# Kernel optimization log

Hardware: AMD Instinct MI355X
Metric: run time of the kernel (lower is better)

Reference implementation:

```python
import jax, jax.numpy as jnp
import numpy as np
from functools import partial

FRAME_RATE = 100
MIN_BPM = 55.0
MAX_BPM = 215.0
THRESHOLD = 0.05
TRANSITION_LAMBDA = 100.0  # madmom-style exponential tempo-change penalty
NEG = jnp.float32(-1e9)


def _build_dbn():
    """Bar-pointer DBN: one block of `tau` phase states per tempo interval tau."""
    min_int = int(round(60.0 * FRAME_RATE / MAX_BPM))
    max_int = int(round(60.0 * FRAME_RATE / MIN_BPM))
    intervals = np.arange(min_int, max_int + 1)              # (T_tempi,)
    state_positions = np.concatenate([np.arange(t) for t in intervals])  # (S,)
    first_idx = np.cumsum(intervals) - intervals             # pos-0 state per tempo
    last_idx = np.cumsum(intervals) - 1                      # last state per tempo
    # exponential tempo-transition distribution, row-normalized in log space
    ratio = intervals[None, :].astype(np.float64) / intervals[:, None]
    raw = -TRANSITION_LAMBDA * np.abs(ratio - 1.0)
    trans_log = raw - np.log(np.exp(raw - raw.max(1, keepdims=True)).sum(1, keepdims=True)) - raw.max(1, keepdims=True)
    return (
        jnp.asarray(state_positions == 0),                    # pos0_mask (S,) bool
        jnp.asarray(first_idx, dtype=jnp.int32),
        jnp.asarray(last_idx, dtype=jnp.int32),
        jnp.asarray(trans_log, dtype=jnp.float32),            # (T_tempi, T_tempi)
    )


def setup_inputs() -> dict:
    key = jax.random.key(0)
    logit = jax.random.normal(key, (4, 6000), dtype=jnp.float32)
    return {"logit": logit}


@jax.jit
def reference(logit):
    pos0_mask, first_idx, last_idx, trans_log = _build_dbn()
    S = pos0_mask.shape[0]
    B, T = logit.shape

    beat_lp = jax.nn.log_sigmoid(logit)      # (B, T)
    nonbeat_lp = jax.nn.log_sigmoid(-logit)  # (B, T)

    def emission(b_t, nb_t):
        # (B, S): beat log-prob on phase-0 states, non-beat elsewhere
        return jnp.where(pos0_mask[None, :], b_t[:, None], nb_t[:, None])

    # ---- Viterbi forward pass with backpointers ----
    def step(delta, xs):
        b_t, nb_t = xs
        prev_last = delta[:, last_idx]                         # (B, T_tempi)
        cand = prev_last[:, :, None] + trans_log[None, :, :]   # (B, from, to)
        from_beat = cand.max(axis=1)                           # (B, T_tempi)
        bp_beat = last_idx[cand.argmax(axis=1)]                # (B, T_tempi)
        # within-tempo advance: state s comes from s-1 (blocks are contiguous)
        shifted = jnp.concatenate(
            [jnp.full((B, 1), NEG, delta.dtype), delta[:, :-1]], axis=1)
        combined = shifted.at[:, first_idx].set(from_beat)
        new_delta = combined + emission(b_t, nb_t)
        bp = jnp.broadcast_to(jnp.arange(S, dtype=jnp.int32) - 1, (B, S))
        bp = bp.at[:, first_idx].set(bp_beat)
        return new_delta, bp

    delta0 = emission(beat_lp[:, 0], nonbeat_lp[:, 0]) - jnp.log(jnp.float32(S))
    xs = (beat_lp[:, 1:].T, nonbeat_lp[:, 1:].T)               # each (T-1, B)
    delta_final, bps = jax.lax.scan(step, delta0, xs)          # bps: (T-1, B, S)

    # ---- backtrack ----
    final_state = jnp.argmax(delta_final, axis=1).astype(jnp.int32)  # (B,)

    def back(state, bp_t):
        prev = jnp.take_along_axis(bp_t, state[:, None], axis=1)[:, 0]
        return prev, state

    state0, ys = jax.lax.scan(back, final_state, bps, reverse=True)
    path = jnp.concatenate([state0[None, :], ys], axis=0)      # (T, B) state ids

    on_beat = pos0_mask[path].T                                # (B, T)
    act = jax.nn.sigmoid(logit)
    beat_mask = on_beat & (act >= jnp.float32(THRESHOLD))
    return beat_mask.astype(jnp.float32)                       # 1.0 at beat frames
```

## Files before the change

### kernel.cpp

```cpp
#include <hip/hip_runtime.h>
#include <math.h>

#define NTAU 82
#define TMIN 28
#define S_TOT 5617
#define TF 6000
#define BATCH 4
#define WMAX 28
#define AP 84
#define NTHREADS 1024
#define NCHUNK 215
#define CHUNK_F (WMAX * AP)
#define NPOS 41

#define TRANS_OFF 0
#define BLP_OFF   8192
#define NBLP_OFF  32768
#define AH_OFF    57344
#define FLAG_OFF  (AH_OFF + BATCH * NCHUNK * CHUNK_F)
#define RESV_OFF  (FLAG_OFF + 16)
#define RESI_OFF  (RESV_OFF + 8)

typedef float v2f __attribute__((ext_vector_type(2)));

__device__ __forceinline__ int first_of(int b) { return b * (55 + b) / 2; }

__device__ __forceinline__ float logsig(float x) {
    return -(fmaxf(-x, 0.0f) + log1pf(expf(-fabsf(x))));
}

__global__ void k_trans(float* __restrict__ ws) {
    int i = blockIdx.x;
    int j = threadIdx.x;
    __shared__ double sh[128];
    double raw = 0.0, e = 0.0;
    double ti = 28.0 + (double)i;
    if (j < NTAU) {
        double tj = 28.0 + (double)j;
        raw = -100.0 * fabs(tj / ti - 1.0);
        e = exp(raw);
    }
    sh[j] = e;
    __syncthreads();
    for (int st = 64; st > 0; st >>= 1) {
        if (j < st) sh[j] += sh[j + st];
        __syncthreads();
    }
    double lse = log(sh[0]);
    if (j < NTAU) ws[TRANS_OFF + i * NTAU + j] = (float)(raw - lse);
}

__global__ void k_emis(const float* __restrict__ logit, float* __restrict__ ws,
                       float* __restrict__ out) {
    int idx = blockIdx.x * blockDim.x + threadIdx.x;
    if (idx < BATCH * TF) {
        float x = logit[idx];
        ws[BLP_OFF + idx]  = logsig(x);
        ws[NBLP_OFF + idx] = logsig(-x);
        out[idx] = 0.0f;
    }
}

__global__ void k_flags(int* __restrict__ flags) {
    if (threadIdx.x < 16) flags[threadIdx.x] = 0;
}

__global__ __attribute__((amdgpu_flat_work_group_size(NTHREADS, NTHREADS),
                          amdgpu_waves_per_eu(4, 4),
                          amdgpu_num_vgpr(128)))
void k_viterbi(const float* __restrict__ logit,
               const float* __restrict__ transg,
               const float* __restrict__ blp_all,
               const float* __restrict__ nblp_all,
               float* __restrict__ Ah_all,
               int*   __restrict__ flags,
               float* __restrict__ resv,
               int*   __restrict__ resi,
               float* __restrict__ out) {
    const int tid = threadIdx.x;
    const int b   = blockIdx.x >> 1;
    const int h   = blockIdx.x & 1;

    const float* blp  = blp_all  + b * TF;
    const float* nblp = nblp_all + b * TF;
    float* Ah = Ah_all + (size_t)b * (NCHUNK * CHUNK_F);
    int* flagOut = flags + b * 2 + h;
    int* flagIn  = flags + b * 2 + (1 - h);

    __shared__ float V[2832];
    __shared__ __align__(16) float A_lds[CHUNK_F];
    __shared__ __align__(16) float fb[CHUNK_F];
    __shared__ __align__(16) float win_nb[4][WMAX];
    __shared__ __align__(16) float win_b[4][WMAX];
    __shared__ float wv[16];
    __shared__ int   wi[16];
    __shared__ int   sstate;

    const int iseg = tid & 3;
    const int jpp  = (tid >> 2) % 21;
    const int tg   = tid / 84;
    const bool p2act = (tid < 1008);
    const int i0 = iseg * 20;
    const int j0 = 4 * jpp + h;
    const bool j1v = (jpp < 20);
    const int j1 = j1v ? (4 * jpp + 2 + h) : j0;

    float tr0[22], tr1[22];
#pragma unroll
    for (int k = 0; k < 22; ++k) { tr0[k] = -1.0e30f; tr1[k] = -1.0e30f; }
    if (p2act) {
        const int icnt = (iseg == 3) ? 22 : 20;
#pragma unroll
        for (int k = 0; k < 22; ++k) {
            if (k < icnt) {
                tr0[k] = transg[(i0 + k) * NTAU + j0];
                if (j1v) tr1[k] = transg[(i0 + k) * NTAU + j1];
            }
        }
    }

    const bool ract = (tid < 1008);
    const int ro = ract ? (tid / 36) : 27;
    const int sp = tid % 36;
    const bool rv2 = ract && (sp < 5);
    const int pA = sp, pB = sp + 36;
    const int colA = 2 * pA + h, colB = 2 * pB + h;
    const int tauA = 28 + 2 * pA + h, tauB = 28 + 2 * pB + h;
    const int foA = pA * (27 + pA + h), foB = pB * (27 + pB + h);
    int rrA = ro, rrB = ro;

    const int NF_TOT = NPOS * (NPOS - 1 + h);
    int nrR[2], nrFo[2], nrTau[2];
    bool nrV[2];
#pragma unroll
    for (int q = 0; q < 2; ++q) {
        const int f = tid + q * NTHREADS;
        nrV[q] = (f < NF_TOT);
        nrR[q] = 28; nrFo[q] = 0; nrTau[q] = 109;
        if (nrV[q]) {
            int lo = 0, hi = NPOS - 1;
            while (lo < hi) { int mid = (lo + hi + 1) >> 1;
                              if (mid * (mid - 1 + h) <= f) lo = mid; else hi = mid - 1; }
            const int m = f - lo * (lo - 1 + h);
            nrR[q]   = TMIN + m;
            nrFo[q]  = lo * (27 + lo + h);
            nrTau[q] = TMIN + 2 * lo + h;
        }
    }

    const int ttI0 = tid / 41, psI0 = tid % 41;
    const int offI0 = ttI0 * AP + 2 * psI0 + (1 - h);
    const bool vI1 = (tid < 124);
    const int ttI1 = (tid + 1024) / 41, psI1 = (tid + 1024) % 41;
    const int offI1 = ttI1 * AP + 2 * psI1 + (1 - h);

    const float logS = (float)log((double)S_TOT);
    const float b0 = blp[0], n0 = nblp[0];
    const int SOWN = NPOS * (68 + h);
    for (int g = tid; g < SOWN; g += NTHREADS) {
        int lo = 0, hi = NPOS - 1;
        while (lo < hi) { int mid = (lo + hi + 1) >> 1;
                          if (mid * (27 + mid + h) <= g) lo = mid; else hi = mid - 1; }
        const int tau = TMIN + 2 * lo + h;
        const int r = g - lo * (27 + lo + h);
        V[g] = ((r == tau - 1) ? b0 : n0) - logS;
    }

    auto winload = [&](int cc) {
        if (cc < NCHUNK && tid < WMAX) {
            int gt = 1 + cc * WMAX + tid;
            win_nb[cc & 3][tid] = (gt < TF) ? nblp[gt] : 0.0f;
            win_b [cc & 3][tid] = (gt < TF) ? blp[gt]  : 0.0f;
        }
    };
    winload(0);
    winload(1);
    __syncthreads();

    float cvA = 0.0f, cvB = 0.0f;
    for (int c = 0; c < NCHUNK; ++c) {
        const int buf = c & 3;
        float* AhC = Ah + (size_t)c * CHUNK_F;

        float nbr[WMAX];
        {
            const float4* wn4 = (const float4*)&win_nb[buf][0];
#pragma unroll
            for (int qq = 0; qq < 7; ++qq) {
                float4 t4 = wn4[qq];
                nbr[4*qq+0] = t4.x; nbr[4*qq+1] = t4.y; nbr[4*qq+2] = t4.z; nbr[4*qq+3] = t4.w;
            }
        }

        cvA = ract ? V[foA + rrA] : 0.0f;
        cvB = rv2  ? V[foB + rrB] : 0.0f;
        for (int tt = 0; tt < ro; ++tt) {
            const float w = win_nb[buf][tt];
            cvA += w; cvB += w;
        }
        if (ract) {
            A_lds[ro * AP + colA] = cvA;
            AhC[ro * AP + colA]   = cvA;
            if (rv2) {
                A_lds[ro * AP + colB] = cvB;
                AhC[ro * AP + colB]   = cvB;
            }
        }
        winload(c + 2);
        __syncthreads();

        if (tid == 0)
            __hip_atomic_fetch_add(flagOut, 1, __ATOMIC_RELEASE, __HIP_MEMORY_SCOPE_AGENT);

        {
            const int a0 = nrFo[0] + nrR[0];
            const int a1 = nrV[1] ? (nrFo[1] + nrR[1]) : a0;
            v2f v01 = v2f{V[a0], V[a1]};
#pragma unroll
            for (int tt = 0; tt < WMAX; ++tt) v01 += v2f{nbr[tt], nbr[tt]};
            V[a0] = v01.x;
            if (nrV[1]) V[a1] = v01.y;
        }

        if (tid == 0) {
            int guard = 0;
            while (__hip_atomic_load(flagIn, __ATOMIC_ACQUIRE, __HIP_MEMORY_SCOPE_AGENT) < c + 1) {
                __builtin_amdgcn_s_sleep(1);
                if (++guard > (1 << 24)) break;
            }
        }
        __syncthreads();

        A_lds[offI0] = AhC[offI0];
        if (vI1) A_lds[offI1] = AhC[offI1];
        __syncthreads();

        if (p2act) {
#pragma unroll
            for (int u = 0; u < 3; ++u) {
                const int tl = tg + 12 * u;
                if (tl < WMAX) {
                    const float4* ar4 = (const float4*)&A_lds[tl * AP + i0];
                    const float4 a0 = ar4[0], a1 = ar4[1], a2 = ar4[2],
                                 a3 = ar4[3], a4 = ar4[4];
                    float m0 = -INFINITY, m1 = -INFINITY;
#define PH2_STEP2(av, aw, ka, kb) { \
    float x0 = (av) + tr0[ka]; float y0 = (aw) + tr0[kb]; \
    m0 = fmaxf(fmaxf(m0, x0), y0); \
    float x1 = (av) + tr1[ka]; float y1 = (aw) + tr1[kb]; \
    m1 = fmaxf(fmaxf(m1, x1), y1); }
                    PH2_STEP2(a0.x, a0.y, 0, 1)   PH2_STEP2(a0.z, a0.w, 2, 3)
                    PH2_STEP2(a1.x, a1.y, 4, 5)   PH2_STEP2(a1.z, a1.w, 6, 7)
                    PH2_STEP2(a2.x, a2.y, 8, 9)   PH2_STEP2(a2.z, a2.w, 10, 11)
                    PH2_STEP2(a3.x, a3.y, 12, 13) PH2_STEP2(a3.z, a3.w, 14, 15)
                    PH2_STEP2(a4.x, a4.y, 16, 17) PH2_STEP2(a4.z, a4.w, 18, 19)
                    if (iseg == 3) {
                        float a20 = A_lds[tl * AP + 80];
                        float a21 = A_lds[tl * AP + 81];
                        PH2_STEP2(a20, a21, 20, 21)
                    }
#undef PH2_STEP2
                    m0 = fmaxf(m0, __shfl_xor(m0, 1)); m1 = fmaxf(m1, __shfl_xor(m1, 1));
                    m0 = fmaxf(m0, __shfl_xor(m0, 2)); m1 = fmaxf(m1, __shfl_xor(m1, 2));
                    if (iseg == 0) {
                        fb[tl * AP + j0] = m0;
                        if (j1v) fb[tl * AP + j1] = m1;
                    }
                }
            }
        }
        __syncthreads();

        {
            const float bw = win_b[buf][ro];
            float eA = ract ? (fb[ro * AP + colA] + bw) : 0.0f;
            float eB = rv2  ? (fb[ro * AP + colB] + bw) : 0.0f;
            for (int tt = ro + 1; tt < WMAX; ++tt) {
                const float w = win_nb[buf][tt];
                eA += w; eB += w;
            }
            const bool keepC = (c == NCHUNK - 1) && (ro >= 7);
            if (ract) {
                V[foA + rrA] = keepC ? cvA : eA;
                if (rv2) V[foB + rrB] = keepC ? cvB : eB;
            }
            rrA += WMAX; if (rrA >= tauA) rrA -= tauA;
            rrB += WMAX; if (rrB >= tauB) rrB -= tauB;
        }
#pragma unroll
        for (int q = 0; q < 2; ++q) {
            if (nrV[q]) { nrR[q] += WMAX; if (nrR[q] >= nrTau[q]) nrR[q] -= nrTau[q]; }
        }
        __syncthreads();
    }

    float bvv = -INFINITY; int bss = 0x7fffffff;
    for (int g = tid; g < SOWN; g += NTHREADS) {
        int lo = 0, hi = NPOS - 1;
        while (lo < hi) { int mid = (lo + hi + 1) >> 1;
                          if (mid * (27 + mid + h) <= g) lo = mid; else hi = mid - 1; }
        const int tau = TMIN + 2 * lo + h;
        const int r = g - lo * (27 + lo + h);
        const int p = (5998 - r) % tau;
        const int s = first_of(2 * lo + h) + p;
        const float v = V[g];
        if (v > bvv || (v == bvv && s < bss)) { bvv = v; bss = s; }
    }
#pragma unroll
    for (int d = 1; d < 64; d <<= 1) {
        float ov = __shfl_xor(bvv, d);
        int   os = __shfl_xor(bss, d);
        if (ov > bvv || (ov == bvv && os < bss)) { bvv = ov; bss = os; }
    }
    if ((tid & 63) == 0) { wv[tid >> 6] = bvv; wi[tid >> 6] = bss; }
    __syncthreads();

    if (tid == 0) {
        float bv = wv[0]; int bs = wi[0];
#pragma unroll
        for (int k = 1; k < 16; ++k) {
            if (wv[k] > bv || (wv[k] == bv && wi[k] < bs)) { bv = wv[k]; bs = wi[k]; }
        }
        resv[b * 2 + h] = bv;
        resi[b * 2 + h] = bs;
        __hip_atomic_fetch_add(flagOut, 1, __ATOMIC_RELEASE, __HIP_MEMORY_SCOPE_AGENT);
        wv[0] = bv; wi[0] = bs;
    }
    if (h == 1) return;
    __syncthreads();

    if (tid == 0) {
        int guard = 0;
        while (__hip_atomic_load(flagIn, __ATOMIC_ACQUIRE, __HIP_MEMORY_SCOPE_AGENT) < NCHUNK + 1) {
            __builtin_amdgcn_s_sleep(1);
            if (++guard > (1 << 26)) break;
        }
        float bv = wv[0]; int bs = wi[0];
        const float pv = resv[b * 2 + 1];
        const int   ps = resi[b * 2 + 1];
        if (pv > bv || (pv == bv && ps < bs)) { bv = pv; bs = ps; }
        sstate = bs;
    }
    __syncthreads();

    if (tid < 64) {
        const int lane = tid;
        int s = sstate;
        int t = TF - 1;
        for (int guard = 0; guard < 400; ++guard) {
            int lo = 0, hi = NTAU - 1;
            while (lo < hi) { int mid = (lo + hi + 1) >> 1;
                              if (first_of(mid) <= s) lo = mid; else hi = mid - 1; }
            int j = lo;
            int p = s - first_of(j);
            int tb = t - p;
            if (tb < 0) break;
            if (lane == 0) {
                float x = logit[b * TF + tb];
                float act = 1.0f / (1.0f + expf(-x));
                if (act >= 0.05f) out[b * TF + tb] = 1.0f;
            }
            if (tb == 0) break;
            const int tq = tb - 1;
            const float* arow = Ah + (size_t)(tq / WMAX) * CHUNK_F + (tq % WMAX) * AP;
            float cvv = arow[lane] + transg[lane * NTAU + j];
            int ci = lane;
            if (lane < NTAU - 64) {
                float c2 = arow[64 + lane] + transg[(64 + lane) * NTAU + j];
                if (c2 > cvv) { cvv = c2; ci = 64 + lane; }
            }
#pragma unroll
            for (int d = 1; d < 64; d <<= 1) {
                float ov = __shfl_xor(cvv, d, 64);
                int   oi = __shfl_xor(ci, d, 64);
                if (ov > cvv || (ov == cvv && oi < ci)) { cvv = ov; ci = oi; }
            }
            s = first_of(ci) + (TMIN + ci) - 1;
            t = tb - 1;
        }
    }
}

extern "C" void kernel_launch(void* const* d_in, const int* in_sizes, int n_in,
                              void* d_out, int out_size, void* d_ws, size_t ws_size,
                              hipStream_t stream) {
    const float* logit = (const float*)d_in[0];
    float* out = (float*)d_out;
    float* ws = (float*)d_ws;
    k_trans<<<dim3(NTAU), dim3(128), 0, stream>>>(ws);
    k_emis<<<dim3((BATCH * TF + 255) / 256), dim3(256), 0, stream>>>(logit, ws, out);
    k_flags<<<dim3(1), dim3(64), 0, stream>>>((int*)(ws + FLAG_OFF));
    k_viterbi<<<dim3(BATCH * 2), dim3(NTHREADS), 0, stream>>>(
        logit, ws + TRANS_OFF, ws + BLP_OFF, ws + NBLP_OFF, ws + AH_OFF,
        (int*)(ws + FLAG_OFF), ws + RESV_OFF, (int*)(ws + RESI_OFF), out);
}
```

Before: 1.398 ms.

## Precompute half of the tempo-transition max before waiting on the partner block

```diff
diff --git a/kernel.cpp b/kernel.cpp
--- a/kernel.cpp
+++ b/kernel.cpp
@@ -177,6 +177,12 @@
     winload(1);
     __syncthreads();
 
+#define PH2_STEP2(av, aw, ka, kb) { \
+    float x0 = (av) + tr0[ka]; float y0 = (aw) + tr0[kb]; \
+    m0 = fmaxf(fmaxf(m0, x0), y0); \
+    float x1 = (av) + tr1[ka]; float y1 = (aw) + tr1[kb]; \
+    m1 = fmaxf(fmaxf(m1, x1), y1); }
+
     float cvA = 0.0f, cvB = 0.0f;
     for (int c = 0; c < NCHUNK; ++c) {
         const int buf = c & 3;
@@ -212,6 +218,40 @@
         if (tid == 0)
             __hip_atomic_fetch_add(flagOut, 1, __ATOMIC_RELEASE, __HIP_MEMORY_SCOPE_AGENT);
 
+        float pm0[3], pm1[3];
+        if (p2act) {
+#pragma unroll
+            for (int u = 0; u < 3; ++u) {
+                const int tl = tg + 12 * u;
+                float m0 = -INFINITY, m1 = -INFINITY;
+                if (tl < WMAX) {
+                    const float4* ar4 = (const float4*)&A_lds[tl * AP + i0];
+                    const float4 a0 = ar4[0], a1 = ar4[1], a2 = ar4[2],
+                                 a3 = ar4[3], a4 = ar4[4];
+                    if (h == 0) {
+                        PH2_STEP2(a0.x, a0.z, 0, 2)   PH2_STEP2(a1.x, a1.z, 4, 6)
+                        PH2_STEP2(a2.x, a2.z, 8, 10)  PH2_STEP2(a3.x, a3.z, 12, 14)
+                        PH2_STEP2(a4.x, a4.z, 16, 18)
+                        if (iseg == 3) {
+                            float a20 = A_lds[tl * AP + 80];
+                            m0 = fmaxf(m0, a20 + tr0[20]);
+                            m1 = fmaxf(m1, a20 + tr1[20]);
+                        }
+                    } else {
+                        PH2_STEP2(a0.y, a0.w, 1, 3)   PH2_STEP2(a1.y, a1.w, 5, 7)
+                        PH2_STEP2(a2.y, a2.w, 9, 11)  PH2_STEP2(a3.y, a3.w, 13, 15)
+                        PH2_STEP2(a4.y, a4.w, 17, 19)
+                        if (iseg == 3) {
+                            float a21 = A_lds[tl * AP + 81];
+                            m0 = fmaxf(m0, a21 + tr0[21]);
+                            m1 = fmaxf(m1, a21 + tr1[21]);
+                        }
+                    }
+                }
+                pm0[u] = m0; pm1[u] = m1;
+            }
+        }
+
         {
             const int a0 = nrFo[0] + nrR[0];
             const int a1 = nrV[1] ? (nrFo[1] + nrR[1]) : a0;
@@ -243,23 +283,26 @@
                     const float4* ar4 = (const float4*)&A_lds[tl * AP + i0];
                     const float4 a0 = ar4[0], a1 = ar4[1], a2 = ar4[2],
                                  a3 = ar4[3], a4 = ar4[4];
-                    float m0 = -INFINITY, m1 = -INFINITY;
-#define PH2_STEP2(av, aw, ka, kb) { \
-    float x0 = (av) + tr0[ka]; float y0 = (aw) + tr0[kb]; \
-    m0 = fmaxf(fmaxf(m0, x0), y0); \
-    float x1 = (av) + tr1[ka]; float y1 = (aw) + tr1[kb]; \
-    m1 = fmaxf(fmaxf(m1, x1), y1); }
-                    PH2_STEP2(a0.x, a0.y, 0, 1)   PH2_STEP2(a0.z, a0.w, 2, 3)
-                    PH2_STEP2(a1.x, a1.y, 4, 5)   PH2_STEP2(a1.z, a1.w, 6, 7)
-                    PH2_STEP2(a2.x, a2.y, 8, 9)   PH2_STEP2(a2.z, a2.w, 10, 11)
-                    PH2_STEP2(a3.x, a3.y, 12, 13) PH2_STEP2(a3.z, a3.w, 14, 15)
-                    PH2_STEP2(a4.x, a4.y, 16, 17) PH2_STEP2(a4.z, a4.w, 18, 19)
-                    if (iseg == 3) {
-                        float a20 = A_lds[tl * AP + 80];
-                        float a21 = A_lds[tl * AP + 81];
-                        PH2_STEP2(a20, a21, 20, 21)
+                    float m0 = pm0[u], m1 = pm1[u];
+                    if (h == 0) {
+                        PH2_STEP2(a0.y, a0.w, 1, 3)   PH2_STEP2(a1.y, a1.w, 5, 7)
+                        PH2_STEP2(a2.y, a2.w, 9, 11)  PH2_STEP2(a3.y, a3.w, 13, 15)
+                        PH2_STEP2(a4.y, a4.w, 17, 19)
+                        if (iseg == 3) {
+                            float a21 = A_lds[tl * AP + 81];
+                            m0 = fmaxf(m0, a21 + tr0[21]);
+                            m1 = fmaxf(m1, a21 + tr1[21]);
+                        }
+                    } else {
+                        PH2_STEP2(a0.x, a0.z, 0, 2)   PH2_STEP2(a1.x, a1.z, 4, 6)
+                        PH2_STEP2(a2.x, a2.z, 8, 10)  PH2_STEP2(a3.x, a3.z, 12, 14)
+                        PH2_STEP2(a4.x, a4.z, 16, 18)
+                        if (iseg == 3) {
+                            float a20 = A_lds[tl * AP + 80];
+                            m0 = fmaxf(m0, a20 + tr0[20]);
+                            m1 = fmaxf(m1, a20 + tr1[20]);
+                        }
                     }
-#undef PH2_STEP2
                     m0 = fmaxf(m0, __shfl_xor(m0, 1)); m1 = fmaxf(m1, __shfl_xor(m1, 1));
                     m0 = fmaxf(m0, __shfl_xor(m0, 2)); m1 = fmaxf(m1, __shfl_xor(m1, 2));
                     if (iseg == 0) {
@@ -293,6 +336,7 @@
         }
         __syncthreads();
     }
+#undef PH2_STEP2
 
     float bvv = -INFINITY; int bss = 0x7fffffff;
     for (int g = tid; g < SOWN; g += NTHREADS) {
```

New measurement: 1.484 ms. +6.1%, slower.

## Fuse phase-2 max with V writeback and let all threads poll the peer flag

Applied to the files above, without the earlier changes.

```diff
diff --git a/kernel.cpp b/kernel.cpp
--- a/kernel.cpp
+++ b/kernel.cpp
@@ -89,7 +89,6 @@
 
     __shared__ float V[2832];
     __shared__ __align__(16) float A_lds[CHUNK_F];
-    __shared__ __align__(16) float fb[CHUNK_F];
     __shared__ __align__(16) float win_nb[4][WMAX];
     __shared__ __align__(16) float win_b[4][WMAX];
     __shared__ float wv[16];
@@ -118,6 +117,15 @@
             }
         }
     }
+
+    const int  jl   = (iseg == 1) ? j1 : j0;
+    const bool wrl  = p2act && ((iseg == 0) || (iseg == 1 && j1v));
+    const int  taul = TMIN + jl;
+    const int  posl = (jl - h) >> 1;
+    const int  fol  = posl * (27 + posl + h);
+    int rl[3];
+#pragma unroll
+    for (int u = 0; u < 3; ++u) rl[u] = tg + 12 * u;
 
     const bool ract = (tid < 1008);
     const int ro = ract ? (tid / 36) : 27;
@@ -177,7 +185,12 @@
     winload(1);
     __syncthreads();
 
-    float cvA = 0.0f, cvB = 0.0f;
+#define PH2_STEP2(av, aw, ka, kb) { \
+    float x0 = (av) + tr0[ka]; float y0 = (aw) + tr0[kb]; \
+    m0 = fmaxf(fmaxf(m0, x0), y0); \
+    float x1 = (av) + tr1[ka]; float y1 = (aw) + tr1[kb]; \
+    m1 = fmaxf(fmaxf(m1, x1), y1); }
+
     for (int c = 0; c < NCHUNK; ++c) {
         const int buf = c & 3;
         float* AhC = Ah + (size_t)c * CHUNK_F;
@@ -192,19 +205,23 @@
             }
         }
 
-        cvA = ract ? V[foA + rrA] : 0.0f;
-        cvB = rv2  ? V[foB + rrB] : 0.0f;
-        for (int tt = 0; tt < ro; ++tt) {
-            const float w = win_nb[buf][tt];
-            cvA += w; cvB += w;
-        }
-        if (ract) {
-            A_lds[ro * AP + colA] = cvA;
-            AhC[ro * AP + colA]   = cvA;
-            if (rv2) {
-                A_lds[ro * AP + colB] = cvB;
-                AhC[ro * AP + colB]   = cvB;
-            }
+        {
+            float cvA = ract ? V[foA + rrA] : 0.0f;
+            float cvB = rv2  ? V[foB + rrB] : 0.0f;
+            for (int tt = 0; tt < ro; ++tt) {
+                const float w = win_nb[buf][tt];
+                cvA += w; cvB += w;
+            }
+            if (ract) {
+                A_lds[ro * AP + colA] = cvA;
+                AhC[ro * AP + colA]   = cvA;
+                if (rv2) {
+                    A_lds[ro * AP + colB] = cvB;
+                    AhC[ro * AP + colB]   = cvB;
+                }
+            }
+            rrA += WMAX; if (rrA >= tauA) rrA -= tauA;
+            rrB += WMAX; if (rrB >= tauB) rrB -= tauB;
         }
         winload(c + 2);
         __syncthreads();
@@ -222,14 +239,15 @@
             if (nrV[1]) V[a1] = v01.y;
         }
 
-        if (tid == 0) {
+        {
             int guard = 0;
-            while (__hip_atomic_load(flagIn, __ATOMIC_ACQUIRE, __HIP_MEMORY_SCOPE_AGENT) < c + 1) {
+            while (__hip_atomic_load(flagIn, __ATOMIC_RELAXED, __HIP_MEMORY_SCOPE_AGENT) < c + 1) {
                 __builtin_amdgcn_s_sleep(1);
                 if (++guard > (1 << 24)) break;
             }
-        }
-        __syncthreads();
+            int fv = __hip_atomic_load(flagIn, __ATOMIC_ACQUIRE, __HIP_MEMORY_SCOPE_AGENT);
+            if (fv < 0) V[0] = -1.0e30f;
+        }
 
         A_lds[offI0] = AhC[offI0];
         if (vI1) A_lds[offI1] = AhC[offI1];
@@ -244,11 +262,6 @@
                     const float4 a0 = ar4[0], a1 = ar4[1], a2 = ar4[2],
                                  a3 = ar4[3], a4 = ar4[4];
                     float m0 = -INFINITY, m1 = -INFINITY;
-#define PH2_STEP2(av, aw, ka, kb) { \
-    float x0 = (av) + tr0[ka]; float y0 = (aw) + tr0[kb]; \
-    m0 = fmaxf(fmaxf(m0, x0), y0); \
-    float x1 = (av) + tr1[ka]; float y1 = (aw) + tr1[kb]; \
-    m1 = fmaxf(fmaxf(m1, x1), y1); }
                     PH2_STEP2(a0.x, a0.y, 0, 1)   PH2_STEP2(a0.z, a0.w, 2, 3)
                     PH2_STEP2(a1.x, a1.y, 4, 5)   PH2_STEP2(a1.z, a1.w, 6, 7)
                     PH2_STEP2(a2.x, a2.y, 8, 9)   PH2_STEP2(a2.z, a2.w, 10, 11)
@@ -259,40 +272,28 @@
                         float a21 = A_lds[tl * AP + 81];
                         PH2_STEP2(a20, a21, 20, 21)
                     }
-#undef PH2_STEP2
                     m0 = fmaxf(m0, __shfl_xor(m0, 1)); m1 = fmaxf(m1, __shfl_xor(m1, 1));
                     m0 = fmaxf(m0, __shfl_xor(m0, 2)); m1 = fmaxf(m1, __shfl_xor(m1, 2));
-                    if (iseg == 0) {
-                        fb[tl * AP + j0] = m0;
-                        if (j1v) fb[tl * AP + j1] = m1;
+                    if (wrl) {
+                        float e = ((iseg == 0) ? m0 : m1) + win_b[buf][tl];
+#pragma unroll
+                        for (int tt = 1; tt < WMAX; ++tt)
+                            e += (tt > tl) ? nbr[tt] : 0.0f;
+                        if (c == NCHUNK - 1 && tl >= 7) e = A_lds[tl * AP + jl];
+                        V[fol + rl[u]] = e;
                     }
+                    rl[u] += WMAX; if (rl[u] >= taul) rl[u] -= taul;
                 }
             }
         }
-        __syncthreads();
-
-        {
-            const float bw = win_b[buf][ro];
-            float eA = ract ? (fb[ro * AP + colA] + bw) : 0.0f;
-            float eB = rv2  ? (fb[ro * AP + colB] + bw) : 0.0f;
-            for (int tt = ro + 1; tt < WMAX; ++tt) {
-                const float w = win_nb[buf][tt];
-                eA += w; eB += w;
-            }
-            const bool keepC = (c == NCHUNK - 1) && (ro >= 7);
-            if (ract) {
-                V[foA + rrA] = keepC ? cvA : eA;
-                if (rv2) V[foB + rrB] = keepC ? cvB : eB;
-            }
-            rrA += WMAX; if (rrA >= tauA) rrA -= tauA;
-            rrB += WMAX; if (rrB >= tauB) rrB -= tauB;
-        }
+
 #pragma unroll
         for (int q = 0; q < 2; ++q) {
             if (nrV[q]) { nrR[q] += WMAX; if (nrR[q] >= nrTau[q]) nrR[q] -= nrTau[q]; }
         }
         __syncthreads();
     }
+#undef PH2_STEP2
 
     float bvv = -INFINITY; int bss = 0x7fffffff;
     for (int g = tid; g < SOWN; g += NTHREADS) {
```

New measurement: 1.710 ms. +22.3%, slower.
